# Kernel optimization log

Hardware: AMD Instinct MI355X
Metric: run time of the kernel (lower is better)

## Reference

```python
import jax, jax.numpy as jnp
import numpy as np

B, S, M, D, H, DH = 2, 1024, 1024, 1024, 16, 64
K = S + M                 # key length
R = 2 * K - 1             # relative position table width
EPS = 1e-5


def layer_norm(x, gamma, beta):
    mu = jnp.mean(x, axis=-1, keepdims=True)
    var = jnp.mean(jnp.square(x - mu), axis=-1, keepdims=True)
    return (x - mu) * jax.lax.rsqrt(var + EPS) * gamma + beta


def skew(q_pos, mem_len):
    # q_pos: (B, H, L, R) with R = 2*k_len - 1
    b, h, L, r = q_pos.shape
    pad = jnp.full((b, h, L, 1), -jnp.inf, q_pos.dtype)
    x = jnp.concatenate([q_pos, pad], axis=-1).reshape(b, h, L * (r + 1))
    x = x[..., : L * r].reshape(b, h, L, r)
    k_len = (r + 1) // 2
    start = k_len - 1 - mem_len
    return x[..., start : start + k_len]  # (B, H, L, k_len)


def setup_inputs() -> dict:
    key = jax.random.key(0)
    ks = jax.random.split(key, 9)
    hidden = jax.random.normal(ks[0], (B, S, D), jnp.float32)
    memory = jax.random.normal(ks[1], (B, M, D), jnp.float32)
    pos_emb = jax.random.normal(ks[2], (B, R, DH), jnp.float32)
    # causal mask: query i may attend keys j <= i + M ; True = blocked
    mask = jnp.arange(K)[None, :] > (jnp.arange(S)[:, None] + M)
    sc = 1.0 / np.sqrt(D)
    Wq = jax.random.normal(ks[3], (D, H * DH), jnp.float32) * sc
    Wk = jax.random.normal(ks[4], (D, H * DH), jnp.float32) * sc
    Wv = jax.random.normal(ks[5], (D, H * DH), jnp.float32) * sc
    Wo = jax.random.normal(ks[6], (H * DH, D), jnp.float32) * sc
    gamma = jnp.ones((D,), jnp.float32)
    beta = jnp.zeros((D,), jnp.float32)
    return {"hidden": hidden, "pos_emb": pos_emb, "memory": memory,
            "mask": mask, "Wq": Wq, "Wk": Wk, "Wv": Wv, "Wo": Wo,
            "gamma": gamma, "beta": beta}


def reference(hidden, pos_emb, memory, mask, Wq, Wk, Wv, Wo, gamma, beta):
    mem_len = memory.shape[1]
    combined = jnp.concatenate([memory, hidden], axis=1)  # (B, K, D)
    h_ln = layer_norm(hidden, gamma, beta)                # pre-LN
    c_ln = layer_norm(combined, gamma, beta)
    q = (h_ln @ Wq).reshape(B, S, H, DH).transpose(0, 2, 1, 3)  # (B,H,S,DH)
    k = (c_ln @ Wk).reshape(B, K, H, DH).transpose(0, 2, 1, 3)  # (B,H,K,DH)
    v = (c_ln @ Wv).reshape(B, K, H, DH).transpose(0, 2, 1, 3)
    score = jnp.einsum('bhsd,bhkd->bhsk', q, k)                  # (B,H,S,K)
    q_pos = jnp.einsum('bhsd,brd->bhsr', q, pos_emb)             # (B,H,S,R)
    score = (score + skew(q_pos, mem_len)) * (1.0 / np.sqrt(D))
    score = jnp.where(mask[None, None], -jnp.inf, score)
    p = jax.nn.softmax(score, axis=-1)
    attn = jnp.einsum('bhsk,bhkd->bshd', p, v).reshape(B, S, H * DH)
    out = attn @ Wo
    return h_ln + out
```

## Files before the change

### kernel.cpp

```cpp
#include <hip/hip_runtime.h>
#include <hip/hip_bf16.h>

#define B_ 2
#define S_ 1024
#define M_ 1024
#define D_ 1024
#define H_ 16
#define DH_ 64
#define K_ 2048
#define R_ 4095

#define NEG_BIG (-1e30f)

typedef unsigned short u16;
typedef short short8 __attribute__((ext_vector_type(8)));
typedef float f32x4 __attribute__((ext_vector_type(4)));

__device__ __forceinline__ u16 f2bf(float f) {
  __hip_bfloat16 h = __float2bfloat16(f);
  return *reinterpret_cast<u16*>(&h);
}
__device__ __forceinline__ float bf2f(u16 u) {
  __hip_bfloat16 h;
  *reinterpret_cast<u16*>(&h) = u;
  return __bfloat162float(h);
}

__device__ __forceinline__ void gll16(const void* g, const void* l) {
  __builtin_amdgcn_global_load_lds(
      (const __attribute__((address_space(1))) unsigned int*)g,
      (__attribute__((address_space(3))) unsigned int*)l, 16, 0, 0);
}

__device__ __forceinline__ f32x4 mfma16(short8 a, short8 b, f32x4 c) {
  return __builtin_amdgcn_mfma_f32_16x16x32_bf16(a, b, c, 0, 0, 0);
}

__global__ __launch_bounds__(256) void prep_kernel(
    const float* __restrict__ hidden, const float* __restrict__ memory,
    const float* __restrict__ gamma, const float* __restrict__ beta,
    u16* __restrict__ cln,
    const float* __restrict__ W0, const float* __restrict__ W1,
    const float* __restrict__ W2, const float* __restrict__ W3,
    u16* __restrict__ O0, u16* __restrict__ O1,
    u16* __restrict__ O2, u16* __restrict__ O3,
    const float* __restrict__ pos, u16* __restrict__ posb) {
  __shared__ u16 tile[64][66];
  __shared__ float red[8];
  const int bx = blockIdx.x;
  const int t = threadIdx.x;

  if (bx < 4096) {
    const int b = bx >> 11;
    const int idx = bx & (K_ - 1);
    const float* src = (idx < M_)
        ? memory + (size_t)(b * M_ + idx) * D_
        : hidden + (size_t)(b * S_ + (idx - M_)) * D_;
    const int lane = t & 63, w = t >> 6;
    float4 rv = ((const float4*)src)[t];
    float s = rv.x + rv.y + rv.z + rv.w;
    float ss = rv.x * rv.x + rv.y * rv.y + rv.z * rv.z + rv.w * rv.w;
#pragma unroll
    for (int m = 1; m < 64; m <<= 1) {
      s += __shfl_xor(s, m, 64);
      ss += __shfl_xor(ss, m, 64);
    }
    if (lane == 0) { red[w] = s; red[4 + w] = ss; }
    __syncthreads();
    s = red[0] + red[1] + red[2] + red[3];
    ss = red[4] + red[5] + red[6] + red[7];
    const float mu = s * (1.0f / D_);
    const float var = ss * (1.0f / D_) - mu * mu;
    const float rstd = rsqrtf(var + 1e-5f);
    float4 gv = ((const float4*)gamma)[t];
    float4 bv = ((const float4*)beta)[t];
    ushort4 ov;
    ov.x = f2bf((rv.x - mu) * rstd * gv.x + bv.x);
    ov.y = f2bf((rv.y - mu) * rstd * gv.y + bv.y);
    ov.z = f2bf((rv.z - mu) * rstd * gv.z + bv.z);
    ov.w = f2bf((rv.w - mu) * rstd * gv.w + bv.w);
    ((ushort4*)(cln + (size_t)bx * D_))[t] = ov;
    return;
  }
  if (bx < 5120) {
    const int z = (bx - 4096) >> 8;
    const int rem = (bx - 4096) & 255;
    const float* in; u16* out;
    switch (z) {
      case 0:  in = W0; out = O0; break;
      case 1:  in = W1; out = O1; break;
      case 2:  in = W2; out = O2; break;
      default: in = W3; out = O3; break;
    }
    const int tx = t & 63, ty = t >> 6;
    const int k0 = (rem & 15) * 64, n0 = (rem >> 4) * 64;
#pragma unroll
    for (int i = ty; i < 64; i += 4)
      tile[i][tx] = f2bf(in[(size_t)(k0 + i) * D_ + n0 + tx]);
    __syncthreads();
#pragma unroll
    for (int i = ty; i < 64; i += 4)
      out[(size_t)(n0 + i) * D_ + k0 + tx] = tile[tx][i];
    return;
  }
  const int i = (bx - 5120) * 256 + t;
  const int n4 = B_ * R_ * 64 / 4;
  if (i < n4) {
    float4 v = ((const float4*)pos)[i];
    ushort4 o;
    o.x = f2bf(v.x); o.y = f2bf(v.y); o.z = f2bf(v.z); o.w = f2bf(v.w);
    ((ushort4*)posb)[i] = o;
  }
}

__device__ __forceinline__ int maprow_hidden(int r) {
  return r + ((r >> 10) << 10) + M_;
}

__global__ __launch_bounds__(256, 3) void gemm_qkv_kernel(
    const u16* __restrict__ A, const u16* __restrict__ Bt,
    u16* __restrict__ qb, u16* __restrict__ kb, u16* __restrict__ vbT) {
  __shared__ __align__(16) u16 As[128 * 64];
  __shared__ __align__(16) u16 Bs[128 * 64];
  const int t = threadIdx.x;
  const int lane = t & 63, w = t >> 6;
  const int wm = w >> 1, wn = w & 1;
  const int qd = lane >> 4, lr = lane & 15;
  const int m0 = blockIdx.y * 128, n0 = blockIdx.x * 128;
  if (n0 < 1024 && !(m0 & 1024)) return;

  const int swz = ((t & 7) ^ ((t >> 3) & 7)) * 8;
  const int c0 = (qd ^ (lr & 7)) * 8;
  const int c1 = c0 ^ 32;
  const int row8 = (t >> 3) & 7;

  f32x4 acc[4][4];
#pragma unroll
  for (int mt = 0; mt < 4; mt++)
#pragma unroll
    for (int nt = 0; nt < 4; nt++) acc[mt][nt] = (f32x4){0.f, 0.f, 0.f, 0.f};

  for (int kt = 0; kt < 1024; kt += 64) {
#pragma unroll
    for (int p = 0; p < 4; p++) {
      const int ra = w * 32 + p * 8 + row8;
      gll16(A + (size_t)(m0 + ra) * 1024 + kt + swz, As + (w * 32 + p * 8) * 64);
      gll16(Bt + (size_t)(n0 + ra) * 1024 + kt + swz, Bs + (w * 32 + p * 8) * 64);
    }
    __syncthreads();
    short8 a0[4], a1[4], b0[4], b1[4];
#pragma unroll
    for (int mt = 0; mt < 4; mt++) {
      a0[mt] = *(const short8*)&As[(wm * 64 + mt * 16 + lr) * 64 + c0];
      a1[mt] = *(const short8*)&As[(wm * 64 + mt * 16 + lr) * 64 + c1];
    }
#pragma unroll
    for (int nt = 0; nt < 4; nt++) {
      b0[nt] = *(const short8*)&Bs[(wn * 64 + nt * 16 + lr) * 64 + c0];
      b1[nt] = *(const short8*)&Bs[(wn * 64 + nt * 16 + lr) * 64 + c1];
    }
#pragma unroll
    for (int mt = 0; mt < 4; mt++)
#pragma unroll
      for (int nt = 0; nt < 4; nt++) {
        acc[mt][nt] = mfma16(a0[mt], b0[nt], acc[mt][nt]);
        acc[mt][nt] = mfma16(a1[mt], b1[nt], acc[mt][nt]);
      }
    __syncthreads();
  }

#pragma unroll
  for (int mt = 0; mt < 4; mt++)
#pragma unroll
    for (int nt = 0; nt < 4; nt++) {
      const int colb = n0 + wn * 64 + nt * 16;
      const int rowb = m0 + wm * 64 + mt * 16 + qd * 4;
      if (colb < 1024) {
        const int qrow = ((rowb >> 11) << 10) | (rowb & 1023);
#pragma unroll
        for (int r = 0; r < 4; r++)
          qb[(size_t)(qrow + r) * 1024 + colb + lr] = f2bf(acc[mt][nt][r] * 0.03125f);
      } else if (colb < 2048) {
        const int key = rowb & (K_ - 1);
        const int bq = rowb >> 11;
#pragma unroll
        for (int r = 0; r < 4; r++)
          kb[(size_t)(bq * K_ + key + r) * 1024 + (colb - 1024) + lr] = f2bf(acc[mt][nt][r]);
      } else {
        const int nn = colb - 2048 + lr;
        const int bh = ((rowb >> 11) << 4) | (nn >> 6);
        const int dh = nn & 63;
        const int key = rowb & (K_ - 1);
        ushort4 pk;
        pk.x = f2bf(acc[mt][nt][0]);
        pk.y = f2bf(acc[mt][nt][1]);
        pk.z = f2bf(acc[mt][nt][2]);
        pk.w = f2bf(acc[mt][nt][3]);
        *(ushort4*)&vbT[((size_t)bh * 64 + dh) * K_ + key] = pk;
      }
    }
}

__global__ __launch_bounds__(256, 2) void out_gemm_kernel(
    const u16* __restrict__ A, const u16* __restrict__ Bt,
    const u16* __restrict__ resid, float* __restrict__ Cf) {
  __shared__ __align__(16) u16 As[128 * 32];
  __shared__ __align__(16) u16 Bs[64 * 32];
  const int t = threadIdx.x;
  const int lane = t & 63, w = t >> 6;
  const int wm = w >> 1, wn = w & 1;
  const int qd = lane >> 4, lr = lane & 15;
  const int m0 = blockIdx.y * 128, n0 = blockIdx.x * 64;

  const u16* Ag0 = A + (size_t)(m0 + (t >> 2)) * 1024 + (t & 3) * 8;
  const u16* Ag1 = Ag0 + (size_t)64 * 1024;
  const u16* Bg0 = Bt + (size_t)(n0 + (t >> 2)) * 1024 + (t & 3) * 8;

  f32x4 acc[4][2];
#pragma unroll
  for (int mt = 0; mt < 4; mt++)
#pragma unroll
    for (int nt = 0; nt < 2; nt++) acc[mt][nt] = (f32x4){0.f, 0.f, 0.f, 0.f};

  for (int kt = 0; kt < 1024; kt += 32) {
    gll16(Ag0 + kt, As + w * 512);
    gll16(Ag1 + kt, As + 2048 + w * 512);
    gll16(Bg0 + kt, Bs + w * 512);
    __syncthreads();
    short8 af[4], bfr[2];
#pragma unroll
    for (int mt = 0; mt < 4; mt++)
      af[mt] = *(const short8*)&As[(wm * 64 + mt * 16 + lr) * 32 + qd * 8];
#pragma unroll
    for (int nt = 0; nt < 2; nt++)
      bfr[nt] = *(const short8*)&Bs[(wn * 32 + nt * 16 + lr) * 32 + qd * 8];
#pragma unroll
    for (int mt = 0; mt < 4; mt++)
#pragma unroll
      for (int nt = 0; nt < 2; nt++)
        acc[mt][nt] = mfma16(af[mt], bfr[nt], acc[mt][nt]);
    __syncthreads();
  }

#pragma unroll
  for (int mt = 0; mt < 4; mt++)
#pragma unroll
    for (int nt = 0; nt < 2; nt++)
#pragma unroll
      for (int r = 0; r < 4; r++) {
        const int row = m0 + wm * 64 + mt * 16 + qd * 4 + r;
        const int col = n0 + wn * 32 + nt * 16 + lr;
        float v = acc[mt][nt][r] + bf2f(resid[(size_t)maprow_hidden(row) * 1024 + col]);
        Cf[(size_t)row * 1024 + col] = v;
      }
}

__global__ __launch_bounds__(256, 2) void attn_kernel(
    const u16* __restrict__ qb, const u16* __restrict__ kb,
    const u16* __restrict__ vbT, const u16* __restrict__ pos,
    u16* __restrict__ ab) {
  __shared__ __align__(16) u16 Ks[2][64 * 64];
  __shared__ __align__(16) u16 Vt[2][64 * 64];
  __shared__ __align__(16) u16 Pt[4][16 * 68];

  const int t = threadIdx.x;
  const int lane = t & 63, w = t >> 6;
  const int qd = lane >> 4, lr = lane & 15;
  const int h = blockIdx.y;
  const int b = blockIdx.z;
  int qt = blockIdx.x;
  if (b) qt = 15 - qt;
  const int i0 = qt * 64;

  const int swz = ((t & 7) ^ ((t >> 3) & 7)) * 8;
  const int c0 = (qd ^ (lr & 7)) * 8;
  const int c1 = c0 ^ 32;
  const int base0 = 960 - i0;
  const int row8 = t >> 3;
  const int bw0 = 48 - w * 16;

  const u16* pb0 = pos + (size_t)(b * R_ + base0 + bw0 + lr) * 64 + qd * 8;

#pragma unroll
  for (int rd = 0; rd < 2; rd++)
    gll16(qb + (size_t)(b * S_ + i0 + rd * 32 + row8) * 1024 + h * 64 + swz,
          &Ks[1][0] + rd * 2048 + w * 512);
#pragma unroll
  for (int rd = 0; rd < 2; rd++) {
    gll16(kb + (size_t)(b * K_ + rd * 32 + row8) * 1024 + h * 64 + swz,
          &Ks[0][0] + rd * 2048 + w * 512);
    gll16(vbT + (size_t)((b * H_ + h) * 64 + rd * 32 + row8) * K_ + swz,
          &Vt[0][0] + rd * 2048 + w * 512);
  }
  short8 pg0[5], pg1[5];
#pragma unroll
  for (int pc = 0; pc < 5; pc++) {
    pg0[pc] = *(const short8*)(pb0 + pc * 1024);
    pg1[pc] = *(const short8*)(pb0 + pc * 1024 + 32);
  }
  __syncthreads();
  const short8 aQ0 = *(const short8*)&Ks[1][(w * 16 + lr) * 64 + c0];
  const short8 aQ1 = *(const short8*)&Ks[1][(w * 16 + lr) * 64 + c1];

  f32x4 accO[4];
#pragma unroll
  for (int d = 0; d < 4; d++) accO[d] = (f32x4){0.f, 0.f, 0.f, 0.f};
  float lsum[4];
#pragma unroll
  for (int r = 0; r < 4; r++) lsum[r] = 0.f;

  const int jmax = min(K_, i0 + 64 + M_);
  int cur = 0;

  for (int j0 = 0, tt = 0; j0 < jmax; j0 += 64, tt++) {
    __syncthreads();
    if (j0 + 64 < jmax) {
      const int nxt = cur ^ 1;
#pragma unroll
      for (int rd = 0; rd < 2; rd++) {
        gll16(kb + (size_t)(b * K_ + j0 + 64 + rd * 32 + row8) * 1024 + h * 64 + swz,
              &Ks[nxt][0] + rd * 2048 + w * 512);
        gll16(vbT + (size_t)((b * H_ + h) * 64 + rd * 32 + row8) * K_ + j0 + 64 + swz,
              &Vt[nxt][0] + rd * 2048 + w * 512);
      }
    }

    f32x4 zp[5];
#pragma unroll
    for (int pc = 0; pc < 5; pc++) {
      f32x4 z = {0.f, 0.f, 0.f, 0.f};
      z = mfma16(aQ0, pg0[pc], z);
      zp[pc] = mfma16(aQ1, pg1[pc], z);
    }

    f32x4 sqk[4];
#pragma unroll
    for (int kc = 0; kc < 4; kc++) {
      const short8 bK0 = *(const short8*)&Ks[cur][(kc * 16 + lr) * 64 + c0];
      const short8 bK1 = *(const short8*)&Ks[cur][(kc * 16 + lr) * 64 + c1];
      f32x4 z = {0.f, 0.f, 0.f, 0.f};
      z = mfma16(aQ0, bK0, z);
      sqk[kc] = mfma16(aQ1, bK1, z);
    }

    {
      const u16* pn = pb0 + (size_t)(tt + 1) * 4096;
#pragma unroll
      for (int pc = 0; pc < 5; pc++) {
        pg0[pc] = *(const short8*)(pn + pc * 1024);
        pg1[pc] = *(const short8*)(pn + pc * 1024 + 32);
      }
    }

    const bool tail = (j0 + 63 > i0 + w * 16 + M_);
    float p[4][4];
#pragma unroll
    for (int r = 0; r < 4; r++) {
      const int iL = qd * 4 + r;
      const int d = 15 + lr - iL;
      const int srcl = qd * 16 + (d & 15);
      const bool hi = (d >> 4) & 1;
      float g0 = __shfl(zp[0][r], srcl, 64);
      float g1 = __shfl(zp[1][r], srcl, 64);
      float g2 = __shfl(zp[2][r], srcl, 64);
      float g3 = __shfl(zp[3][r], srcl, 64);
      float g4 = __shfl(zp[4][r], srcl, 64);
      float s0 = sqk[0][r] + (hi ? g1 : g0);
      float s1 = sqk[1][r] + (hi ? g2 : g1);
      float s2 = sqk[2][r] + (hi ? g3 : g2);
      float s3 = sqk[3][r] + (hi ? g4 : g3);
      if (tail) {
        const int key = j0 + lr, lim = i0 + w * 16 + iL + M_;
        if (key      > lim) s0 = NEG_BIG;
        if (key + 16 > lim) s1 = NEG_BIG;
        if (key + 32 > lim) s2 = NEG_BIG;
        if (key + 48 > lim) s3 = NEG_BIG;
      }
      p[0][r] = __expf(s0);
      p[1][r] = __expf(s1);
      p[2][r] = __expf(s2);
      p[3][r] = __expf(s3);
      lsum[r] += p[0][r] + p[1][r] + p[2][r] + p[3][r];
    }

#pragma unroll
    for (int r = 0; r < 4; r++) {
      const int base = (qd * 4 + r) * 68 + lr;
      Pt[w][base +  0] = f2bf(p[0][r]);
      Pt[w][base + 16] = f2bf(p[1][r]);
      Pt[w][base + 32] = f2bf(p[2][r]);
      Pt[w][base + 48] = f2bf(p[3][r]);
    }
    __asm__ volatile("s_waitcnt lgkmcnt(0)" ::: "memory");
    const short8 aP0 = *(const short8*)&Pt[w][lr * 68 + qd * 8];
    const short8 aP1 = *(const short8*)&Pt[w][lr * 68 + 32 + qd * 8];

#pragma unroll
    for (int d2 = 0; d2 < 4; d2++) {
      const short8 bV0 = *(const short8*)&Vt[cur][(d2 * 16 + lr) * 64 + c0];
      const short8 bV1 = *(const short8*)&Vt[cur][(d2 * 16 + lr) * 64 + c1];
      accO[d2] = mfma16(aP0, bV0, accO[d2]);
      accO[d2] = mfma16(aP1, bV1, accO[d2]);
    }

    cur ^= 1;
  }

  float inv[4];
#pragma unroll
  for (int r = 0; r < 4; r++) {
#pragma unroll
    for (int msk = 1; msk < 16; msk <<= 1) lsum[r] += __shfl_xor(lsum[r], msk, 64);
    inv[r] = 1.0f / lsum[r];
  }
#pragma unroll
  for (int d2 = 0; d2 < 4; d2++)
#pragma unroll
    for (int r = 0; r < 4; r++) {
      const int iG = i0 + w * 16 + qd * 4 + r;
      ab[(size_t)(b * S_ + iG) * 1024 + h * 64 + d2 * 16 + lr] = f2bf(accO[d2][r] * inv[r]);
    }
}

extern "C" void kernel_launch(void* const* d_in, const int* in_sizes, int n_in,
                              void* d_out, int out_size, void* d_ws, size_t ws_size,
                              hipStream_t stream) {
  const float* hidden = (const float*)d_in[0];
  const float* pos    = (const float*)d_in[1];
  const float* memory = (const float*)d_in[2];
  const float* Wq = (const float*)d_in[4];
  const float* Wk = (const float*)d_in[5];
  const float* Wv = (const float*)d_in[6];
  const float* Wo = (const float*)d_in[7];
  const float* gamma = (const float*)d_in[8];
  const float* beta  = (const float*)d_in[9];

  char* ws = (char*)d_ws;
  u16* cln  = (u16*)(ws);
  u16* qb   = (u16*)(ws + 8388608);
  u16* kb   = (u16*)(ws + 12582912);
  u16* vbT  = (u16*)(ws + 20971520);
  u16* ab   = (u16*)(ws + 29360128);
  u16* WqT  = (u16*)(ws + 33554432);
  u16* WkT  = WqT + 1048576;
  u16* WvT  = WkT + 1048576;
  u16* WoT  = WvT + 1048576;
  u16* posb = (u16*)(ws + 41943040);

  prep_kernel<<<dim3(5632), 256, 0, stream>>>(
      hidden, memory, gamma, beta, cln,
      Wq, Wk, Wv, Wo, WqT, WkT, WvT, WoT, pos, posb);
  gemm_qkv_kernel<<<dim3(24, 32), 256, 0, stream>>>(cln, WqT, qb, kb, vbT);
  attn_kernel<<<dim3(S_ / 64, H_, B_), 256, 0, stream>>>(qb, kb, vbT, posb, ab);
  out_gemm_kernel<<<dim3(16, 16), 256, 0, stream>>>(ab, WoT, cln, (float*)d_out);
}
```

Before: 219.8 us.

## Split attention key range across two blocks and combine with atomics

Each query tile's key loop is split into two halves processed by separate blocks. Partial unnormalized outputs and row sums are accumulated with float atomicAdd into zeroed fp32 buffers, and a new combine kernel normalizes them and writes bf16. The intent is more parallelism and occupancy (launch bounds raised to 4, grid doubled), and a swizzled P-tile layout is used to avoid LDS bank conflicts. In exchange it adds atomic traffic, an extra zeroing pass in prep, and an extra kernel launch. It relies on there being no running-max rescaling, so summing partials without a max is valid.

Result: slower. 322.6 us (+46.8%).

```diff
diff --git a/kernel.cpp b/kernel.cpp
--- a/kernel.cpp
+++ b/kernel.cpp
@@ -44,7 +44,8 @@
     const float* __restrict__ W2, const float* __restrict__ W3,
     u16* __restrict__ O0, u16* __restrict__ O1,
     u16* __restrict__ O2, u16* __restrict__ O3,
-    const float* __restrict__ pos, u16* __restrict__ posb) {
+    const float* __restrict__ pos, u16* __restrict__ posb,
+    float* __restrict__ accb, float* __restrict__ lsumb) {
   __shared__ u16 tile[64][66];
   __shared__ float red[8];
   const int bx = blockIdx.x;
@@ -103,13 +104,22 @@
       out[(size_t)(n0 + i) * D_ + k0 + tx] = tile[tx][i];
     return;
   }
-  const int i = (bx - 5120) * 256 + t;
-  const int n4 = B_ * R_ * 64 / 4;
-  if (i < n4) {
-    float4 v = ((const float4*)pos)[i];
-    ushort4 o;
-    o.x = f2bf(v.x); o.y = f2bf(v.y); o.z = f2bf(v.z); o.w = f2bf(v.w);
-    ((ushort4*)posb)[i] = o;
+  if (bx < 5632) {
+    const int i = (bx - 5120) * 256 + t;
+    const int n4 = B_ * R_ * 64 / 4;
+    if (i < n4) {
+      float4 v = ((const float4*)pos)[i];
+      ushort4 o;
+      o.x = f2bf(v.x); o.y = f2bf(v.y); o.z = f2bf(v.z); o.w = f2bf(v.w);
+      ((ushort4*)posb)[i] = o;
+    }
+    return;
+  }
+  {
+    const int i = (bx - 5632) * 256 + t;
+    const float4 z4 = {0.f, 0.f, 0.f, 0.f};
+    if (i < 524288) ((float4*)accb)[i] = z4;
+    else ((float4*)lsumb)[i - 524288] = z4;
   }
 }
 
@@ -255,21 +265,21 @@
       }
 }
 
-__global__ __launch_bounds__(256, 2) void attn_kernel(
+__global__ __launch_bounds__(256, 4) void attn_kernel(
     const u16* __restrict__ qb, const u16* __restrict__ kb,
     const u16* __restrict__ vbT, const u16* __restrict__ pos,
-    u16* __restrict__ ab) {
+    float* __restrict__ accb, float* __restrict__ lsumb) {
   __shared__ __align__(16) u16 Ks[2][64 * 64];
   __shared__ __align__(16) u16 Vt[2][64 * 64];
-  __shared__ __align__(16) u16 Pt[4][16 * 68];
+  __shared__ __align__(16) u16 Pt[4][16 * 64];
 
   const int t = threadIdx.x;
   const int lane = t & 63, w = t >> 6;
   const int qd = lane >> 4, lr = lane & 15;
   const int h = blockIdx.y;
   const int b = blockIdx.z;
-  int qt = blockIdx.x;
-  if (b) qt = 15 - qt;
+  const int qt = blockIdx.x & 15;
+  const int half = blockIdx.x >> 4;
   const int i0 = qt * 64;
 
   const int swz = ((t & 7) ^ ((t >> 3) & 7)) * 8;
@@ -279,6 +289,14 @@
   const int row8 = t >> 3;
   const int bw0 = 48 - w * 16;
 
+  const int jmax = min(K_, i0 + 64 + M_);
+  const int nt_total = jmax >> 6;
+  const int nt0 = nt_total >> 1;
+  const int t_start = half ? nt0 : 0;
+  const int t_end = half ? nt_total : nt0;
+  const int j0s = t_start * 64;
+  const int jend = t_end * 64;
+
   const u16* pb0 = pos + (size_t)(b * R_ + base0 + bw0 + lr) * 64 + qd * 8;
 
 #pragma unroll
@@ -287,16 +305,19 @@
           &Ks[1][0] + rd * 2048 + w * 512);
 #pragma unroll
   for (int rd = 0; rd < 2; rd++) {
-    gll16(kb + (size_t)(b * K_ + rd * 32 + row8) * 1024 + h * 64 + swz,
+    gll16(kb + (size_t)(b * K_ + j0s + rd * 32 + row8) * 1024 + h * 64 + swz,
           &Ks[0][0] + rd * 2048 + w * 512);
-    gll16(vbT + (size_t)((b * H_ + h) * 64 + rd * 32 + row8) * K_ + swz,
+    gll16(vbT + (size_t)((b * H_ + h) * 64 + rd * 32 + row8) * K_ + j0s + swz,
           &Vt[0][0] + rd * 2048 + w * 512);
   }
   short8 pg0[5], pg1[5];
-#pragma unroll
-  for (int pc = 0; pc < 5; pc++) {
-    pg0[pc] = *(const short8*)(pb0 + pc * 1024);
-    pg1[pc] = *(const short8*)(pb0 + pc * 1024 + 32);
+  {
+    const u16* pp = pb0 + (size_t)t_start * 4096;
+#pragma unroll
+    for (int pc = 0; pc < 5; pc++) {
+      pg0[pc] = *(const short8*)(pp + pc * 1024);
+      pg1[pc] = *(const short8*)(pp + pc * 1024 + 32);
+    }
   }
   __syncthreads();
   const short8 aQ0 = *(const short8*)&Ks[1][(w * 16 + lr) * 64 + c0];
@@ -309,12 +330,11 @@
 #pragma unroll
   for (int r = 0; r < 4; r++) lsum[r] = 0.f;
 
-  const int jmax = min(K_, i0 + 64 + M_);
   int cur = 0;
 
-  for (int j0 = 0, tt = 0; j0 < jmax; j0 += 64, tt++) {
-    __syncthreads();
-    if (j0 + 64 < jmax) {
+  for (int j0 = j0s, tt = t_start; j0 < jend; j0 += 64, tt++) {
+    __syncthreads();
+    if (j0 + 64 < jend) {
       const int nxt = cur ^ 1;
 #pragma unroll
       for (int rd = 0; rd < 2; rd++) {
@@ -385,15 +405,17 @@
 
 #pragma unroll
     for (int r = 0; r < 4; r++) {
-      const int base = (qd * 4 + r) * 68 + lr;
-      Pt[w][base +  0] = f2bf(p[0][r]);
-      Pt[w][base + 16] = f2bf(p[1][r]);
-      Pt[w][base + 32] = f2bf(p[2][r]);
-      Pt[w][base + 48] = f2bf(p[3][r]);
+      const int row = qd * 4 + r;
+      const int cbase = row * 64;
+      const int rx = row & 7;
+      const int lo = lr & 7, hi8 = lr >> 3;
+#pragma unroll
+      for (int kc = 0; kc < 4; kc++)
+        Pt[w][cbase + ((((kc << 1) | hi8) ^ rx) << 3) + lo] = f2bf(p[kc][r]);
     }
     __asm__ volatile("s_waitcnt lgkmcnt(0)" ::: "memory");
-    const short8 aP0 = *(const short8*)&Pt[w][lr * 68 + qd * 8];
-    const short8 aP1 = *(const short8*)&Pt[w][lr * 68 + 32 + qd * 8];
+    const short8 aP0 = *(const short8*)&Pt[w][lr * 64 + ((qd ^ (lr & 7)) << 3)];
+    const short8 aP1 = *(const short8*)&Pt[w][lr * 64 + (((qd + 4) ^ (lr & 7)) << 3)];
 
 #pragma unroll
     for (int d2 = 0; d2 < 4; d2++) {
@@ -406,20 +428,45 @@
     cur ^= 1;
   }
 
-  float inv[4];
 #pragma unroll
   for (int r = 0; r < 4; r++) {
 #pragma unroll
     for (int msk = 1; msk < 16; msk <<= 1) lsum[r] += __shfl_xor(lsum[r], msk, 64);
-    inv[r] = 1.0f / lsum[r];
-  }
-#pragma unroll
-  for (int d2 = 0; d2 < 4; d2++)
+  }
+  if (lr == 0) {
 #pragma unroll
     for (int r = 0; r < 4; r++) {
       const int iG = i0 + w * 16 + qd * 4 + r;
-      ab[(size_t)(b * S_ + iG) * 1024 + h * 64 + d2 * 16 + lr] = f2bf(accO[d2][r] * inv[r]);
-    }
+      atomicAdd(&lsumb[(b * H_ + h) * S_ + iG], lsum[r]);
+    }
+  }
+#pragma unroll
+  for (int d2 = 0; d2 < 4; d2++)
+#pragma unroll
+    for (int r = 0; r < 4; r++) {
+      const int iG = i0 + w * 16 + qd * 4 + r;
+      atomicAdd(&accb[(size_t)(b * S_ + iG) * 1024 + h * 64 + d2 * 16 + lr],
+                accO[d2][r]);
+    }
+}
+
+__global__ __launch_bounds__(256) void combine_kernel(
+    const float* __restrict__ accb, const float* __restrict__ lsumb,
+    u16* __restrict__ ab) {
+  const int idx = blockIdx.x * 256 + threadIdx.x;
+  const float4 a = ((const float4*)accb)[idx];
+  const int flat = idx << 2;
+  const int bcol = flat & 1023;
+  const int i = (flat >> 10) & (S_ - 1);
+  const int b = flat >> 20;
+  const int h = bcol >> 6;
+  const float inv = 1.0f / lsumb[(b * H_ + h) * S_ + i];
+  ushort4 o;
+  o.x = f2bf(a.x * inv);
+  o.y = f2bf(a.y * inv);
+  o.z = f2bf(a.z * inv);
+  o.w = f2bf(a.w * inv);
+  ((ushort4*)ab)[idx] = o;
 }
 
 extern "C" void kernel_launch(void* const* d_in, const int* in_sizes, int n_in,
@@ -446,11 +493,14 @@
   u16* WvT  = WkT + 1048576;
   u16* WoT  = WvT + 1048576;
   u16* posb = (u16*)(ws + 41943040);
-
-  prep_kernel<<<dim3(5632), 256, 0, stream>>>(
+  float* accb  = (float*)(ws + 44040192);
+  float* lsumb = (float*)(ws + 52428800);
+
+  prep_kernel<<<dim3(7712), 256, 0, stream>>>(
       hidden, memory, gamma, beta, cln,
-      Wq, Wk, Wv, Wo, WqT, WkT, WvT, WoT, pos, posb);
+      Wq, Wk, Wv, Wo, WqT, WkT, WvT, WoT, pos, posb, accb, lsumb);
   gemm_qkv_kernel<<<dim3(24, 32), 256, 0, stream>>>(cln, WqT, qb, kb, vbT);
-  attn_kernel<<<dim3(S_ / 64, H_, B_), 256, 0, stream>>>(qb, kb, vbT, posb, ab);
+  attn_kernel<<<dim3(32, H_, B_), 256, 0, stream>>>(qb, kb, vbT, posb, accb, lsumb);
+  combine_kernel<<<dim3(2048), 256, 0, stream>>>(accb, lsumb, ab);
   out_gemm_kernel<<<dim3(16, 16), 256, 0, stream>>>(ab, WoT, cln, (float*)d_out);
 }
```
